# Kernel optimization log

Hardware: AMD Instinct MI355X
Metric: run time of the kernel (lower is better)

The kernel has to match this reference:

```python
import jax, jax.numpy as jnp
import numpy as np

B = 64          # graphs per batch
NN = 4096       # nodes per graph (64x64 lattice)
N = B * NN      # total nodes
DEG = 4         # avg degree
E = N * DEG     # total directed edges
DIN, H, L = 1, 128, 64


def setup_inputs() -> dict:
    key = jax.random.key(0)
    ks = jax.random.split(key, 16)
    x = jax.random.normal(ks[0], (N, DIN), dtype=jnp.float32)
    eps = jax.random.normal(ks[1], (B, L), dtype=jnp.float32)
    # per-graph random edges, offset so they never cross graphs
    src = jax.random.randint(ks[2], (E,), 0, NN)
    dst = jax.random.randint(ks[3], (E,), 0, NN)
    off = (jnp.arange(E) // (NN * DEG)) * NN
    edge_index = jnp.stack([src + off, dst + off]).astype(jnp.int32)
    batch = (jnp.arange(N) // NN).astype(jnp.int32)
    s = 0.02
    p = lambda k, shp: s * jax.random.normal(k, shp, dtype=jnp.float32)
    return {
        "x": x, "eps": eps,
        "enc_w1": p(ks[4], (DIN, H)), "enc_b1": jnp.zeros((H,), jnp.float32),
        "enc_w2": p(ks[5], (H, H)),   "enc_b2": jnp.zeros((H,), jnp.float32),
        "mu_w": p(ks[6], (H, L)),     "mu_b": jnp.zeros((L,), jnp.float32),
        "lv_w": p(ks[7], (H, L)),     "lv_b": jnp.zeros((L,), jnp.float32),
        "zn_w": p(ks[8], (L, H)),     "zn_b": jnp.zeros((H,), jnp.float32),
        "dec_w1": p(ks[9], (H, H)),   "dec_b1": jnp.zeros((H,), jnp.float32),
        "dec_w2": p(ks[10], (H, H)),  "dec_b2": jnp.zeros((H,), jnp.float32),
        "out_w": p(ks[11], (H, 1)),   "out_b": jnp.zeros((1,), jnp.float32),
        "edge_index": edge_index, "batch": batch,
    }


def _gcn(h, w, b, row, col, norm, n):
    # PyG GCNConv: xW -> gather at row, scale by sym-norm, scatter-sum at col, + bias
    hw = h @ w
    msg = hw[row] * norm[:, None]
    return jax.ops.segment_sum(msg, col, num_segments=n) + b


def reference(x, eps, enc_w1, enc_b1, enc_w2, enc_b2, mu_w, mu_b, lv_w, lv_b,
              zn_w, zn_b, dec_w1, dec_b1, dec_w2, dec_b2, out_w, out_b,
              edge_index, batch):
    n = x.shape[0]
    b = eps.shape[0]
    nn_ = n // b
    # add self-loops, symmetric GCN normalization (shared by all convs)
    loops = jnp.arange(n, dtype=edge_index.dtype)
    row = jnp.concatenate([edge_index[0], loops])
    col = jnp.concatenate([edge_index[1], loops])
    deg = jax.ops.segment_sum(jnp.ones_like(col, dtype=x.dtype), col, num_segments=n)
    dinv = jnp.where(deg > 0, jax.lax.rsqrt(deg), 0.0)
    norm = dinv[row] * dinv[col]
    h = jax.nn.relu(_gcn(x, enc_w1, enc_b1, row, col, norm, n))
    h = jax.nn.relu(_gcn(h, enc_w2, enc_b2, row, col, norm, n))
    cnt = jax.ops.segment_sum(jnp.ones((n,), x.dtype), batch, num_segments=b)
    hg = jax.ops.segment_sum(h, batch, num_segments=b) / cnt[:, None]
    mu = hg @ mu_w + mu_b
    logvar = hg @ lv_w + lv_b
    # ---- reparameterize ----
    z = mu + jnp.exp(0.5 * logvar) * eps
    zn = z @ zn_w + zn_b          # [B, H]
    hd = zn[batch]                # [N, H]
    hd = jax.nn.relu(_gcn(hd, dec_w1, dec_b1, row, col, norm, n))
    hd = jax.nn.relu(_gcn(hd, dec_w2, dec_b2, row, col, norm, n))
    spin = jnp.tanh(hd @ out_w + out_b)   # [N, 1]
    recon = spin.reshape(b, nn_)
    return (recon, mu, logvar, z)
```

## Files before the change

kernel.cpp:

```cpp
#include <hip/hip_runtime.h>
#include <math.h>

#define NTOT 262144
#define BG   64
#define NNPG 4096
#define ET   1048576
#define EPG  16384
#define EPB  4096
#define HD   128
#define LD   64
#define NSEG 129
#define TN   256
#define MCAP ET

__device__ __forceinline__ void swz(int b, int& g, int& j){
  int xcd = b & 7, q = b >> 3;
  g = (q >> 2)*8 + xcd;
  j = q & 3;
}

__global__ void __launch_bounds__(1024) k_count(const int* __restrict__ ei,
                                                int* __restrict__ cntJ){
  __shared__ int h[NNPG];
  int g, j; swz(blockIdx.x, g, j);
  int tid = threadIdx.x;
  #pragma unroll
  for (int k = tid; k < NNPG; k += 1024) h[k] = 0;
  __syncthreads();
  int gbase = g*NNPG;
  const int4* dsts4 = (const int4*)(ei + ET + g*EPG + j*EPB);
  int4 D = dsts4[tid];
  atomicAdd(&h[D.x - gbase], 1); atomicAdd(&h[D.y - gbase], 1);
  atomicAdd(&h[D.z - gbase], 1); atomicAdd(&h[D.w - gbase], 1);
  __syncthreads();
  int* plane = cntJ + j*NTOT + gbase;
  #pragma unroll
  for (int k = tid; k < NNPG; k += 1024) plane[k] = h[k];
}

__global__ void k_dinvxd(const int* __restrict__ cntJ, const float* __restrict__ x,
                         float2* __restrict__ xd){
  int i = blockIdx.x*256 + threadIdx.x;
  int deg = cntJ[i] + cntJ[NTOT+i] + cntJ[2*NTOT+i] + cntJ[3*NTOT+i];
  xd[i] = make_float2(x[i], rsqrtf((float)deg + 1.0f));
}

__global__ void __launch_bounds__(128) k_tab1a(
    const float* __restrict__ w1, const float* __restrict__ b1,
    float* __restrict__ t1, int* __restrict__ nfp){
  __shared__ int ks[128];
  int j = threadIdx.x;
  float w = w1[j], b = b1[j];
  float t; int kind;
  if (w != 0.0f){ t = -b / w; kind = (w > 0.0f) ? 0 : 1; }
  else          { t = INFINITY; kind = 2; }
  ks[j] = kind;
  t1[j] = t;
  __syncthreads();
  if (j == 0){
    int c = 0;
    for (int q = 0; q < 128; q++) c += (ks[q] != 2) ? 1 : 0;
    nfp[0] = c;
  }
}

__global__ void __launch_bounds__(1024) k_edge1(
    const int* __restrict__ ei, const float2* __restrict__ xd,
    float2* __restrict__ accJ)
{
  __shared__ float ax[NNPG];
  __shared__ float s1[NNPG];
  int tid = threadIdx.x;
  int g, j; swz(blockIdx.x, g, j);
  int gbase = g*NNPG;
  const int4* srcs4 = (const int4*)(ei + g*EPG + j*EPB);
  const int4* dsts4 = (const int4*)(ei + ET + g*EPG + j*EPB);
  int4 S = srcs4[tid], D = dsts4[tid];
  *(float4*)(ax + 4*tid) = make_float4(0.f,0.f,0.f,0.f);
  *(float4*)(s1 + 4*tid) = make_float4(0.f,0.f,0.f,0.f);
  __syncthreads();
  #define P1(s_, d_) { float2 sd = xd[s_]; int dl = (d_) - gbase; \
    atomicAdd(&ax[dl], sd.y * sd.x); \
    atomicAdd(&s1[dl], sd.y); }
  P1(S.x, D.x); P1(S.y, D.y); P1(S.z, D.z); P1(S.w, D.w);
  #undef P1
  __syncthreads();
  float4* ap = (float4*)(accJ + (size_t)j*NTOT + gbase);
  ap[2*tid+0] = make_float4(ax[4*tid+0], s1[4*tid+0], ax[4*tid+1], s1[4*tid+1]);
  ap[2*tid+1] = make_float4(ax[4*tid+2], s1[4*tid+2], ax[4*tid+3], s1[4*tid+3]);
}

__global__ void k_pack(const float2* __restrict__ xd, const float2* __restrict__ accJ,
                       const float* __restrict__ t1,
                       float4* __restrict__ rec, float* __restrict__ srowA,
                       int* __restrict__ segU1){
  __shared__ float ts[128];
  __shared__ int used[8];
  int tid = threadIdx.x;
  if (tid < 128) ts[tid] = t1[tid];
  if (tid < 8) used[tid] = 0;
  __syncthreads();
  int i = blockIdx.x*256 + tid;
  float2 xdv = xd[i];
  float2 a0 = accJ[0*NTOT + i], a1 = accJ[1*NTOT + i];
  float2 a2 = accJ[2*NTOT + i], a3 = accJ[3*NTOT + i];
  float axs = (a0.x + a1.x) + (a2.x + a3.x);
  float s1s = (a0.y + a1.y) + (a2.y + a3.y);
  float di = xdv.y;
  float ax = di * (di * xdv.x + axs);
  float sr = di * (di + s1s);
  int sc = 0;
  for (int q = 0; q < 128; q++) sc += (ts[q] < ax) ? 1 : 0;
  rec[i] = make_float4(di, di*ax, di*sr, __int_as_float(sc));
  srowA[i] = sr;
  atomicOr(&used[sc>>5], 1u << (sc & 31));
  __syncthreads();
  if (tid < 8 && used[tid]) atomicOr(&segU1[tid], used[tid]);
}

__global__ void __launch_bounds__(1024) k_tabrows(
    const float* __restrict__ wsrc, const float* __restrict__ bsrc,
    const float* __restrict__ w2, const int* __restrict__ segUsed,
    const int* __restrict__ nfA, float* __restrict__ ACbase)
{
  __shared__ float ws[128], bs[128], tsh[128];
  __shared__ int ks[128], rr[128];
  __shared__ float red[8][128][4];
  int g = blockIdx.x;
  int tid = threadIdx.x;
  int k = tid & 127, qg = tid >> 7;
  if (qg == 0){
    float w = wsrc[g*HD + k], b = bsrc[k];
    float t; int kind;
    if (w != 0.0f){ t = -b / w; kind = (w > 0.0f) ? 0 : 1; }
    else          { t = INFINITY; kind = 2; }
    ws[k] = w; bs[k] = b; tsh[k] = t; ks[k] = kind;
  }
  __syncthreads();
  if (qg == 0){
    float t = tsh[k];
    int r = 0;
    for (int q = 0; q < 128; q++){
      if (ks[q] != 2){
        float tq = tsh[q];
        if (tq < t || (tq == t && q < k)) r++;
      }
    }
    rr[k] = r;
  }
  float a0=0.f, c0=0.f, an=0.f, cn=0.f;
  #pragma unroll
  for (int u = 0; u < 16; u++){
    int q = qg*16 + u;
    float v = w2[q*HD + k];
    int kd = ks[q];
    float wq = ws[q], bq = bs[q];
    bool m0 = (kd == 1) || (kd == 2 && bq > 0.f);
    bool mn = (kd == 0) || (kd == 2 && bq > 0.f);
    float wv = wq*v, bv = bq*v;
    a0 += m0 ? wv : 0.f; c0 += m0 ? bv : 0.f;
    an += mn ? wv : 0.f; cn += mn ? bv : 0.f;
  }
  red[qg][k][0]=a0; red[qg][k][1]=c0; red[qg][k][2]=an; red[qg][k][3]=cn;
  __syncthreads();
  int nf = nfA[g];
  float* ACg = ACbase + (size_t)g*NSEG*256;
  int base = (k>>2)*8 + (k&3);
  if (qg == 0){
    float A0=0.f,C0=0.f,An=0.f,Cn=0.f;
    #pragma unroll
    for (int p = 0; p < 8; p++){
      A0+=red[p][k][0]; C0+=red[p][k][1]; An+=red[p][k][2]; Cn+=red[p][k][3];
    }
    ACg[base] = A0; ACg[base+4] = C0;
    ACg[(size_t)nf*256 + base] = An; ACg[(size_t)nf*256 + base + 4] = Cn;
  }
  __syncthreads();
  for (int wd = 0; wd < 5; wd++){
    unsigned m = (unsigned)segUsed[g*8 + wd];
    if (wd == 0) m &= ~1u;
    if ((nf >> 5) == wd) m &= ~(1u << (nf & 31));
    while (m){
      int bit = __ffs(m) - 1;
      m &= m - 1;
      int s = wd*32 + bit;
      float pa=0.f, pc=0.f;
      #pragma unroll
      for (int u = 0; u < 16; u++){
        int q = qg*16 + u;
        int kd = ks[q];
        bool act = (kd == 0) ? (rr[q] < s) : (kd == 1) ? (rr[q] >= s) : (bs[q] > 0.f);
        float v = act ? w2[q*HD + k] : 0.f;
        pa = fmaf(ws[q], v, pa); pc = fmaf(bs[q], v, pc);
      }
      red[qg][k][0]=pa; red[qg][k][1]=pc;
      __syncthreads();
      if (qg == 0){
        float A=0.f,C=0.f;
        #pragma unroll
        for (int p = 0; p < 8; p++){ A+=red[p][k][0]; C+=red[p][k][1]; }
        ACg[(size_t)s*256 + base] = A; ACg[(size_t)s*256 + base + 4] = C;
      }
      __syncthreads();
    }
  }
}

__global__ void __launch_bounds__(1024) k_edge2enc(
    const int* __restrict__ ei, const float4* __restrict__ rec,
    const int* __restrict__ nfp, float4* __restrict__ sums4,
    int2* __restrict__ missL, int* __restrict__ mcnt)
{
  __shared__ float sf[NNPG*4];
  int g, j; swz(blockIdx.x, g, j);
  int tid = threadIdx.x;
  int gbase = g*NNPG;
  int nf = nfp[0];
  const int4* srcs4 = (const int4*)(ei + g*EPG + j*EPB);
  const int4* dsts4 = (const int4*)(ei + ET + g*EPG + j*EPB);
  int4 S = srcs4[tid], D = dsts4[tid];
  float4* sf4 = (float4*)sf;
  #pragma unroll
  for (int k = 0; k < 4; k++) sf4[4*tid + k] = make_float4(0.f,0.f,0.f,0.f);
  __syncthreads();
  #define E1(s_, d_) { float4 r = rec[s_]; int dl = (d_) - gbase; \
    int sb = __float_as_int(r.w); \
    atomicAdd(&sf[dl*4+0], r.y); atomicAdd(&sf[dl*4+1], r.x); \
    if (sb == nf) { atomicAdd(&sf[dl*4+2], r.y); atomicAdd(&sf[dl*4+3], r.x); } \
    else if (sb != 0) { int ix = atomicAdd(&mcnt[0], 1); \
      if (ix < MCAP) missL[ix] = make_int2(d_, s_); } }
  E1(S.x, D.x); E1(S.y, D.y); E1(S.z, D.z); E1(S.w, D.w);
  #undef E1
  __syncthreads();
  float4* sp = sums4 + (size_t)j*NTOT + gbase;
  #pragma unroll
  for (int k = 0; k < 4; k++) sp[4*tid + k] = sf4[4*tid + k];
}

__global__ void __launch_bounds__(256) k_enc_fin(
    const float4* __restrict__ rec, const float4* __restrict__ sums4,
    const float4* __restrict__ AC, const float* __restrict__ b2,
    const int* __restrict__ nfp, const int2* __restrict__ missL,
    const int* __restrict__ mcnt, float* __restrict__ hgsum)
{
  __shared__ float4 sS[TN];
  __shared__ float4 sRA[TN];
  __shared__ float red[256*4];
  int bid = blockIdx.x, g = bid & 63, part = bid >> 6;
  int tid = threadIdx.x, lane = tid & 31, nrow = tid >> 5;
  int base = g*NNPG + part*TN;
  int nf = nfp[0];
  {
    int i = base + tid;
    sRA[tid] = rec[i];
    float4 a = sums4[0*NTOT + i], b = sums4[1*NTOT + i];
    float4 c = sums4[2*NTOT + i], d = sums4[3*NTOT + i];
    sS[tid] = make_float4(a.x+b.x+c.x+d.x, a.y+b.y+c.y+d.y,
                          a.z+b.z+c.z+d.z, a.w+b.w+c.w+d.w);
  }
  __syncthreads();
  const float4* q0 = AC + (size_t)lane*2;
  const float4* qn = AC + ((size_t)nf*32 + lane)*2;
  float4 A0 = q0[0], C0 = q0[1], An = qn[0], Cn = qn[1];
  float4 dA = make_float4(An.x-A0.x, An.y-A0.y, An.z-A0.z, An.w-A0.w);
  float4 dC = make_float4(Cn.x-C0.x, Cn.y-C0.y, Cn.z-C0.z, Cn.w-C0.w);
  float4 bb = ((const float4*)b2)[lane];
  int mc = mcnt[0]; mc = mc < MCAP ? mc : MCAP;
  float gx=0.f, gy=0.f, gz=0.f, gw=0.f;
  for (int it = 0; it < TN/8; ++it){
    int li = it*8 + nrow;
    int i = base + li;
    float4 rA = sRA[li];
    float4 s4 = sS[li];
    float accx = fmaf(s4.x,A0.x, fmaf(s4.z,dA.x, fmaf(s4.y,C0.x, s4.w*dC.x)));
    float accy = fmaf(s4.x,A0.y, fmaf(s4.z,dA.y, fmaf(s4.y,C0.y, s4.w*dC.y)));
    float accz = fmaf(s4.x,A0.z, fmaf(s4.z,dA.z, fmaf(s4.y,C0.z, s4.w*dC.z)));
    float accw = fmaf(s4.x,A0.w, fmaf(s4.z,dA.w, fmaf(s4.y,C0.w, s4.w*dC.w)));
    if (mc > 0){
      for (int e = 0; e < mc; e++){
        int2 me = missL[e];
        if (me.x == i){
          float4 r = rec[me.y];
          int sb = __float_as_int(r.w);
          const float4* qm = AC + ((size_t)sb*32 + lane)*2;
          float4 qa = qm[0], qc = qm[1];
          accx = fmaf(r.y, qa.x-A0.x, fmaf(r.x, qc.x-C0.x, accx));
          accy = fmaf(r.y, qa.y-A0.y, fmaf(r.x, qc.y-C0.y, accy));
          accz = fmaf(r.y, qa.z-A0.z, fmaf(r.x, qc.z-C0.z, accz));
          accw = fmaf(r.y, qa.w-A0.w, fmaf(r.x, qc.w-C0.w, accw));
        }
      }
    }
    int si = __float_as_int(rA.w);
    bool m0 = (si == 0);
    float4 sa, sc;
    sa.x = m0 ? A0.x : An.x; sa.y = m0 ? A0.y : An.y; sa.z = m0 ? A0.z : An.z; sa.w = m0 ? A0.w : An.w;
    sc.x = m0 ? C0.x : Cn.x; sc.y = m0 ? C0.y : Cn.y; sc.z = m0 ? C0.z : Cn.z; sc.w = m0 ? C0.w : Cn.w;
    if (si != 0 && si != nf){
      const float4* qs = AC + ((size_t)si*32 + lane)*2;
      sa = qs[0]; sc = qs[1];
    }
    float d = rA.x, d2 = d*d, ca = rA.y*d;
    gx += fmaxf(fmaf(d, accx, fmaf(ca, sa.x, d2*sc.x)) + bb.x, 0.f);
    gy += fmaxf(fmaf(d, accy, fmaf(ca, sa.y, d2*sc.y)) + bb.y, 0.f);
    gz += fmaxf(fmaf(d, accz, fmaf(ca, sa.z, d2*sc.z)) + bb.z, 0.f);
    gw += fmaxf(fmaf(d, accw, fmaf(ca, sa.w, d2*sc.w)) + bb.w, 0.f);
  }
  __syncthreads();
  red[tid*4+0] = gx; red[tid*4+1] = gy; red[tid*4+2] = gz; red[tid*4+3] = gw;
  __syncthreads();
  if (nrow == 0){
    float tx=0.f, ty=0.f, tz=0.f, tw=0.f;
    for (int r2 = 0; r2 < 8; r2++){
      int t2 = (r2*32 + lane)*4;
      tx += red[t2]; ty += red[t2+1]; tz += red[t2+2]; tw += red[t2+3];
    }
    atomicAdd(&hgsum[g*HD + lane*4 + 0], tx);
    atomicAdd(&hgsum[g*HD + lane*4 + 1], ty);
    atomicAdd(&hgsum[g*HD + lane*4 + 2], tz);
    atomicAdd(&hgsum[g*HD + lane*4 + 3], tw);
  }
}

__global__ void __launch_bounds__(128) k_small(
    const float* __restrict__ hgsum,
    const float* __restrict__ mu_w, const float* __restrict__ mu_b,
    const float* __restrict__ lv_w, const float* __restrict__ lv_b,
    const float* __restrict__ eps,
    const float* __restrict__ zn_w, const float* __restrict__ zn_b,
    const float* __restrict__ dec_w1, const float* __restrict__ dec_b1,
    float* __restrict__ out_mu, float* __restrict__ out_lv, float* __restrict__ out_z,
    float* __restrict__ t2, float* __restrict__ ushG, int* __restrict__ nf2)
{
  int g = blockIdx.x, tid = threadIdx.x;
  __shared__ float hg[128], zsh[64], znsh[128];
  __shared__ int ks[128];
  hg[tid] = hgsum[g*HD + tid] * (1.0f/4096.0f);
  __syncthreads();
  if (tid < 64){
    int l = tid;
    float m = mu_b[l], v = lv_b[l];
    for (int k = 0; k < HD; k++){
      float hv = hg[k];
      m = fmaf(hv, mu_w[k*LD + l], m);
      v = fmaf(hv, lv_w[k*LD + l], v);
    }
    int o = g*LD + l;
    out_mu[o] = m; out_lv[o] = v;
    float zv = fmaf(expf(0.5f*v), eps[o], m);
    out_z[o] = zv; zsh[l] = zv;
  }
  __syncthreads();
  {
    int k = tid;
    float acc = zn_b[k];
    for (int l = 0; l < LD; l++) acc = fmaf(zsh[l], zn_w[l*HD + k], acc);
    znsh[k] = acc;
  }
  __syncthreads();
  float w;
  {
    int k = tid;
    float acc = 0.f;
    for (int j = 0; j < HD; j++) acc = fmaf(znsh[j], dec_w1[j*HD + k], acc);
    ushG[g*HD + k] = acc;
    w = acc;
  }
  float b = dec_b1[tid];
  float t; int kind;
  if (w != 0.0f){ t = -b / w; kind = (w > 0.0f) ? 0 : 1; }
  else          { t = INFINITY; kind = 2; }
  t2[g*HD + tid] = t; ks[tid] = kind;
  __syncthreads();
  if (tid == 0){
    int c = 0;
    for (int q = 0; q < 128; q++) c += (ks[q] != 2) ? 1 : 0;
    nf2[g] = c;
  }
}

__global__ void k_seg2(const float* __restrict__ t2, const float* __restrict__ srowA,
                       float4* __restrict__ rec, int* __restrict__ segUsed){
  __shared__ float ts[128];
  __shared__ int used[8];
  int tid = threadIdx.x;
  int i = blockIdx.x*256 + tid;
  int g = blockIdx.x >> 4;
  if (tid < 128) ts[tid] = t2[g*HD + tid];
  if (tid < 8) used[tid] = 0;
  __syncthreads();
  float a = srowA[i];
  int sc = 0;
  for (int q = 0; q < 128; q++) sc += (ts[q] < a) ? 1 : 0;
  float4 r = rec[i];
  r.y = __int_as_float(sc);
  rec[i] = r;
  atomicOr(&used[sc>>5], 1u << (sc & 31));
  __syncthreads();
  if (tid < 8 && used[tid]) atomicOr(&segUsed[g*8 + tid], used[tid]);
}

__global__ void __launch_bounds__(1024) k_edge2dec(
    const int* __restrict__ ei, const float4* __restrict__ rec,
    const int* __restrict__ nf2, float4* __restrict__ sums4,
    int2* __restrict__ missL, int* __restrict__ mcnt)
{
  __shared__ float sf[NNPG*4];
  int g, j; swz(blockIdx.x, g, j);
  int tid = threadIdx.x;
  int gbase = g*NNPG;
  int nf = nf2[g];
  const int4* srcs4 = (const int4*)(ei + g*EPG + j*EPB);
  const int4* dsts4 = (const int4*)(ei + ET + g*EPG + j*EPB);
  int4 S = srcs4[tid], D = dsts4[tid];
  float4* sf4 = (float4*)sf;
  #pragma unroll
  for (int k = 0; k < 4; k++) sf4[4*tid + k] = make_float4(0.f,0.f,0.f,0.f);
  __syncthreads();
  #define E2(s_, d_) { float4 r = rec[s_]; int dl = (d_) - gbase; \
    int sb = __float_as_int(r.y); \
    atomicAdd(&sf[dl*4+0], r.z); atomicAdd(&sf[dl*4+1], r.x); \
    if (sb == nf) { atomicAdd(&sf[dl*4+2], r.z); atomicAdd(&sf[dl*4+3], r.x); } \
    else if (sb != 0) { int ix = atomicAdd(&mcnt[1], 1); \
      if (ix < MCAP) missL[ix] = make_int2(d_, s_); } }
  E2(S.x, D.x); E2(S.y, D.y); E2(S.z, D.z); E2(S.w, D.w);
  #undef E2
  __syncthreads();
  float4* sp = sums4 + (size_t)j*NTOT + gbase;
  #pragma unroll
  for (int k = 0; k < 4; k++) sp[4*tid + k] = sf4[4*tid + k];
}

__global__ void __launch_bounds__(256) k_dec_fin(
    const float4* __restrict__ rec, const float4* __restrict__ sums4,
    const float4* __restrict__ AC2, const float* __restrict__ b2,
    const float* __restrict__ ow, const float* __restrict__ ob,
    const int* __restrict__ nf2, const int2* __restrict__ missL,
    const int* __restrict__ mcnt, float* __restrict__ recon)
{
  __shared__ float4 sS[TN];
  __shared__ float4 sRA[TN];
  int bid = blockIdx.x, g = bid & 63, part = bid >> 6;
  int tid = threadIdx.x, lane = tid & 31, nrow = tid >> 5;
  int base = g*NNPG + part*TN;
  int nf = nf2[g];
  const float4* AC = AC2 + (size_t)g*NSEG*64;
  {
    int i = base + tid;
    sRA[tid] = rec[i];
    float4 a = sums4[0*NTOT + i], b = sums4[1*NTOT + i];
    float4 c = sums4[2*NTOT + i], d = sums4[3*NTOT + i];
    sS[tid] = make_float4(a.x+b.x+c.x+d.x, a.y+b.y+c.y+d.y,
                          a.z+b.z+c.z+d.z, a.w+b.w+c.w+d.w);
  }
  __syncthreads();
  const float4* q0 = AC + (size_t)lane*2;
  const float4* qn = AC + ((size_t)nf*32 + lane)*2;
  float4 A0 = q0[0], C0 = q0[1], An = qn[0], Cn = qn[1];
  float4 dA = make_float4(An.x-A0.x, An.y-A0.y, An.z-A0.z, An.w-A0.w);
  float4 dC = make_float4(Cn.x-C0.x, Cn.y-C0.y, Cn.z-C0.z, Cn.w-C0.w);
  float4 bb  = ((const float4*)b2)[lane];
  float4 owv = ((const float4*)ow)[lane];
  float obv = ob[0];
  int mc = mcnt[1]; mc = mc < MCAP ? mc : MCAP;
  for (int it = 0; it < TN/8; ++it){
    int li = it*8 + nrow;
    int i = base + li;
    float4 rA = sRA[li];
    float4 s4 = sS[li];
    float accx = fmaf(s4.x,A0.x, fmaf(s4.z,dA.x, fmaf(s4.y,C0.x, s4.w*dC.x)));
    float accy = fmaf(s4.x,A0.y, fmaf(s4.z,dA.y, fmaf(s4.y,C0.y, s4.w*dC.y)));
    float accz = fmaf(s4.x,A0.z, fmaf(s4.z,dA.z, fmaf(s4.y,C0.z, s4.w*dC.z)));
    float accw = fmaf(s4.x,A0.w, fmaf(s4.z,dA.w, fmaf(s4.y,C0.w, s4.w*dC.w)));
    if (mc > 0){
      for (int e = 0; e < mc; e++){
        int2 me = missL[e];
        if (me.x == i){
          float4 r = rec[me.y];
          int sb = __float_as_int(r.y);
          const float4* qm = AC + ((size_t)sb*32 + lane)*2;
          float4 qa = qm[0], qc = qm[1];
          accx = fmaf(r.z, qa.x-A0.x, fmaf(r.x, qc.x-C0.x, accx));
          accy = fmaf(r.z, qa.y-A0.y, fmaf(r.x, qc.y-C0.y, accy));
          accz = fmaf(r.z, qa.z-A0.z, fmaf(r.x, qc.z-C0.z, accz));
          accw = fmaf(r.z, qa.w-A0.w, fmaf(r.x, qc.w-C0.w, accw));
        }
      }
    }
    int si = __float_as_int(rA.y);
    bool m0 = (si == 0);
    float4 sa, sc;
    sa.x = m0 ? A0.x : An.x; sa.y = m0 ? A0.y : An.y; sa.z = m0 ? A0.z : An.z; sa.w = m0 ? A0.w : An.w;
    sc.x = m0 ? C0.x : Cn.x; sc.y = m0 ? C0.y : Cn.y; sc.z = m0 ? C0.z : Cn.z; sc.w = m0 ? C0.w : Cn.w;
    if (si != 0 && si != nf){
      const float4* qs = AC + ((size_t)si*32 + lane)*2;
      sa = qs[0]; sc = qs[1];
    }
    float d = rA.x, d2 = d*d, ca = rA.z*d;
    float hx = fmaxf(fmaf(d, accx, fmaf(ca, sa.x, d2*sc.x)) + bb.x, 0.f);
    float hy = fmaxf(fmaf(d, accy, fmaf(ca, sa.y, d2*sc.y)) + bb.y, 0.f);
    float hz = fmaxf(fmaf(d, accz, fmaf(ca, sa.z, d2*sc.z)) + bb.z, 0.f);
    float hw = fmaxf(fmaf(d, accw, fmaf(ca, sa.w, d2*sc.w)) + bb.w, 0.f);
    float dsum = hx*owv.x + hy*owv.y + hz*owv.z + hw*owv.w;
    for (int o2 = 16; o2 > 0; o2 >>= 1) dsum += __shfl_down(dsum, o2, 32);
    if (lane == 0) recon[i] = tanhf(dsum + obv);
  }
}

extern "C" void kernel_launch(void* const* d_in, const int* in_sizes, int n_in,
                              void* d_out, int out_size, void* d_ws, size_t ws_size,
                              hipStream_t stream){
  (void)in_sizes; (void)n_in; (void)out_size; (void)ws_size;
  const float* x      = (const float*)d_in[0];
  const float* eps    = (const float*)d_in[1];
  const float* enc_w1 = (const float*)d_in[2];
  const float* enc_b1 = (const float*)d_in[3];
  const float* enc_w2 = (const float*)d_in[4];
  const float* enc_b2 = (const float*)d_in[5];
  const float* mu_w   = (const float*)d_in[6];
  const float* mu_b   = (const float*)d_in[7];
  const float* lv_w   = (const float*)d_in[8];
  const float* lv_b   = (const float*)d_in[9];
  const float* zn_w   = (const float*)d_in[10];
  const float* zn_b   = (const float*)d_in[11];
  const float* dec_w1 = (const float*)d_in[12];
  const float* dec_b1 = (const float*)d_in[13];
  const float* dec_w2 = (const float*)d_in[14];
  const float* dec_b2 = (const float*)d_in[15];
  const float* out_w  = (const float*)d_in[16];
  const float* out_b  = (const float*)d_in[17];
  const int*   ei     = (const int*)d_in[18];

  float* out       = (float*)d_out;
  float* out_recon = out;
  float* out_mu    = out + NTOT;
  float* out_lv    = out_mu + BG*LD;
  float* out_z     = out_lv + BG*LD;

  char* w = (char*)d_ws;
  size_t off_b = 0;
  auto alloc = [&](size_t bytes)->void*{
    void* p = w + off_b;
    off_b += (bytes + 255) & ~(size_t)255;
    return p;
  };
  char*   regA   = (char*) alloc((size_t)4*NTOT*16);
  int*    cntJ   = (int*)   regA;
  float2* accJ   = (float2*)(regA + (size_t)4*NTOT*4);
  float4* sums4  = (float4*)regA;
  float2* xd     = (float2*)alloc((size_t)NTOT*8);
  float4* rec    = (float4*)alloc((size_t)NTOT*16);
  float*  srowA  = (float*) alloc((size_t)NTOT*4);
  int2*   missL  = (int2*)  alloc((size_t)MCAP*8);
  float*  t1     = (float*) alloc(128*4);
  int*    nf1    = (int*)   alloc(256);
  int*    nf2    = (int*)   alloc(BG*4);
  int*    segU1  = (int*)   alloc(8*4);
  int*    segU   = (int*)   alloc(BG*8*4);
  float*  t2     = (float*) alloc((size_t)BG*HD*4);
  float*  ushG   = (float*) alloc((size_t)BG*HD*4);
  float*  AC1    = (float*) alloc((size_t)NSEG*256*4);
  float*  AC2    = (float*) alloc((size_t)BG*NSEG*256*4);
  float*  hgsum  = (float*) alloc((size_t)BG*HD*4 + 256);
  int*    mcnt   = (int*)(hgsum + BG*HD);

  hipMemsetAsync(hgsum, 0, (size_t)BG*HD*4 + 256, stream);
  hipMemsetAsync(segU1, 0, 8*4, stream);
  hipMemsetAsync(segU,  0, (size_t)BG*8*4, stream);

  k_tab1a <<<1, 128, 0, stream>>>(enc_w1, enc_b1, t1, nf1);
  k_count <<<256, 1024, 0, stream>>>(ei, cntJ);
  k_dinvxd<<<NTOT/256, 256, 0, stream>>>(cntJ, x, xd);
  k_edge1 <<<256, 1024, 0, stream>>>(ei, xd, accJ);
  k_pack  <<<NTOT/256, 256, 0, stream>>>(xd, accJ, t1, rec, srowA, segU1);
  k_tabrows<<<1, 1024, 0, stream>>>(enc_w1, enc_b1, enc_w2, segU1, nf1, AC1);

  k_edge2enc<<<256, 1024, 0, stream>>>(ei, rec, nf1, sums4, missL, mcnt);
  k_enc_fin <<<1024, 256, 0, stream>>>(rec, sums4, (const float4*)AC1, enc_b2,
                                       nf1, missL, mcnt, hgsum);

  k_small<<<BG, 128, 0, stream>>>(hgsum, mu_w, mu_b, lv_w, lv_b, eps,
                                  zn_w, zn_b, dec_w1, dec_b1,
                                  out_mu, out_lv, out_z, t2, ushG, nf2);

  k_seg2<<<NTOT/256, 256, 0, stream>>>(t2, srowA, rec, segU);

  k_tabrows<<<BG, 1024, 0, stream>>>(ushG, dec_b1, dec_w2, segU, nf2, AC2);

  k_edge2dec<<<256, 1024, 0, stream>>>(ei, rec, nf2, sums4, missL, mcnt);
  k_dec_fin <<<1024, 256, 0, stream>>>(rec, sums4, (const float4*)AC2, dec_b2,
                                       out_w, out_b, nf2, missL, mcnt, out_recon);
}
```

Measured before the change: 177.9 us.

## Fuse setup memsets and small kernels, stage per-graph node records in LDS

```diff
diff --git a/kernel.cpp b/kernel.cpp
--- a/kernel.cpp
+++ b/kernel.cpp
@@ -20,10 +20,36 @@
 }
 
 __global__ void __launch_bounds__(1024) k_count(const int* __restrict__ ei,
-                                                int* __restrict__ cntJ){
+                                                const float* __restrict__ w1,
+                                                const float* __restrict__ b1,
+                                                int* __restrict__ cntJ,
+                                                float* __restrict__ t1, int* __restrict__ nfp,
+                                                float* __restrict__ hgsum,
+                                                int* __restrict__ mcnt,
+                                                int* __restrict__ segU1){
   __shared__ int h[NNPG];
+  int tid = threadIdx.x;
+  if (blockIdx.x == 256){
+    for (int idx = tid; idx < BG*HD; idx += 1024) hgsum[idx] = 0.f;
+    if (tid < 2) mcnt[tid] = 0;
+    if (tid < 8) segU1[tid] = 0;
+    if (tid < 128){
+      float w = w1[tid], b = b1[tid];
+      float t; int kind;
+      if (w != 0.0f){ t = -b / w; kind = (w > 0.0f) ? 0 : 1; }
+      else          { t = INFINITY; kind = 2; }
+      h[tid] = kind;
+      t1[tid] = t;
+    }
+    __syncthreads();
+    if (tid == 0){
+      int c = 0;
+      for (int q = 0; q < 128; q++) c += (h[q] != 2) ? 1 : 0;
+      nfp[0] = c;
+    }
+    return;
+  }
   int g, j; swz(blockIdx.x, g, j);
-  int tid = threadIdx.x;
   #pragma unroll
   for (int k = tid; k < NNPG; k += 1024) h[k] = 0;
   __syncthreads();
@@ -43,25 +69,6 @@
   int i = blockIdx.x*256 + threadIdx.x;
   int deg = cntJ[i] + cntJ[NTOT+i] + cntJ[2*NTOT+i] + cntJ[3*NTOT+i];
   xd[i] = make_float2(x[i], rsqrtf((float)deg + 1.0f));
-}
-
-__global__ void __launch_bounds__(128) k_tab1a(
-    const float* __restrict__ w1, const float* __restrict__ b1,
-    float* __restrict__ t1, int* __restrict__ nfp){
-  __shared__ int ks[128];
-  int j = threadIdx.x;
-  float w = w1[j], b = b1[j];
-  float t; int kind;
-  if (w != 0.0f){ t = -b / w; kind = (w > 0.0f) ? 0 : 1; }
-  else          { t = INFINITY; kind = 2; }
-  ks[j] = kind;
-  t1[j] = t;
-  __syncthreads();
-  if (j == 0){
-    int c = 0;
-    for (int q = 0; q < 128; q++) c += (ks[q] != 2) ? 1 : 0;
-    nfp[0] = c;
-  }
 }
 
 __global__ void __launch_bounds__(1024) k_edge1(
@@ -212,6 +219,7 @@
     int2* __restrict__ missL, int* __restrict__ mcnt)
 {
   __shared__ float sf[NNPG*4];
+  __shared__ float4 sRec[NNPG];
   int g, j; swz(blockIdx.x, g, j);
   int tid = threadIdx.x;
   int gbase = g*NNPG;
@@ -221,9 +229,12 @@
   int4 S = srcs4[tid], D = dsts4[tid];
   float4* sf4 = (float4*)sf;
   #pragma unroll
-  for (int k = 0; k < 4; k++) sf4[4*tid + k] = make_float4(0.f,0.f,0.f,0.f);
-  __syncthreads();
-  #define E1(s_, d_) { float4 r = rec[s_]; int dl = (d_) - gbase; \
+  for (int k = 0; k < 4; k++){
+    sf4[4*tid + k] = make_float4(0.f,0.f,0.f,0.f);
+    sRec[k*1024 + tid] = rec[gbase + k*1024 + tid];
+  }
+  __syncthreads();
+  #define E1(s_, d_) { float4 r = sRec[(s_) - gbase]; int dl = (d_) - gbase; \
     int sb = __float_as_int(r.w); \
     atomicAdd(&sf[dl*4+0], r.y); atomicAdd(&sf[dl*4+1], r.x); \
     if (sb == nf) { atomicAdd(&sf[dl*4+2], r.y); atomicAdd(&sf[dl*4+3], r.x); } \
@@ -322,20 +333,24 @@
   }
 }
 
-__global__ void __launch_bounds__(128) k_small(
+__global__ void __launch_bounds__(1024) k_small(
     const float* __restrict__ hgsum,
     const float* __restrict__ mu_w, const float* __restrict__ mu_b,
     const float* __restrict__ lv_w, const float* __restrict__ lv_b,
     const float* __restrict__ eps,
     const float* __restrict__ zn_w, const float* __restrict__ zn_b,
     const float* __restrict__ dec_w1, const float* __restrict__ dec_b1,
+    const float* __restrict__ srowA,
     float* __restrict__ out_mu, float* __restrict__ out_lv, float* __restrict__ out_z,
-    float* __restrict__ t2, float* __restrict__ ushG, int* __restrict__ nf2)
+    float* __restrict__ ushG, int* __restrict__ nf2,
+    float4* __restrict__ rec, int* __restrict__ segUsed)
 {
   int g = blockIdx.x, tid = threadIdx.x;
   __shared__ float hg[128], zsh[64], znsh[128];
-  __shared__ int ks[128];
-  hg[tid] = hgsum[g*HD + tid] * (1.0f/4096.0f);
+  __shared__ float ts[128];
+  __shared__ int ks[128], used[8];
+  if (tid < 128) hg[tid] = hgsum[g*HD + tid] * (1.0f/4096.0f);
+  if (tid < 8) used[tid] = 0;
   __syncthreads();
   if (tid < 64){
     int l = tid;
@@ -351,53 +366,42 @@
     out_z[o] = zv; zsh[l] = zv;
   }
   __syncthreads();
-  {
-    int k = tid;
-    float acc = zn_b[k];
-    for (int l = 0; l < LD; l++) acc = fmaf(zsh[l], zn_w[l*HD + k], acc);
-    znsh[k] = acc;
-  }
-  __syncthreads();
-  float w;
-  {
-    int k = tid;
+  if (tid < 128){
+    float acc = zn_b[tid];
+    for (int l = 0; l < LD; l++) acc = fmaf(zsh[l], zn_w[l*HD + tid], acc);
+    znsh[tid] = acc;
+  }
+  __syncthreads();
+  if (tid < 128){
     float acc = 0.f;
-    for (int j = 0; j < HD; j++) acc = fmaf(znsh[j], dec_w1[j*HD + k], acc);
-    ushG[g*HD + k] = acc;
-    w = acc;
-  }
-  float b = dec_b1[tid];
-  float t; int kind;
-  if (w != 0.0f){ t = -b / w; kind = (w > 0.0f) ? 0 : 1; }
-  else          { t = INFINITY; kind = 2; }
-  t2[g*HD + tid] = t; ks[tid] = kind;
+    for (int j = 0; j < HD; j++) acc = fmaf(znsh[j], dec_w1[j*HD + tid], acc);
+    ushG[g*HD + tid] = acc;
+    float b = dec_b1[tid];
+    float t; int kind;
+    if (acc != 0.0f){ t = -b / acc; kind = (acc > 0.0f) ? 0 : 1; }
+    else            { t = INFINITY; kind = 2; }
+    ts[tid] = t; ks[tid] = kind;
+  }
   __syncthreads();
   if (tid == 0){
     int c = 0;
     for (int q = 0; q < 128; q++) c += (ks[q] != 2) ? 1 : 0;
     nf2[g] = c;
   }
-}
-
-__global__ void k_seg2(const float* __restrict__ t2, const float* __restrict__ srowA,
-                       float4* __restrict__ rec, int* __restrict__ segUsed){
-  __shared__ float ts[128];
-  __shared__ int used[8];
-  int tid = threadIdx.x;
-  int i = blockIdx.x*256 + tid;
-  int g = blockIdx.x >> 4;
-  if (tid < 128) ts[tid] = t2[g*HD + tid];
-  if (tid < 8) used[tid] = 0;
-  __syncthreads();
-  float a = srowA[i];
-  int sc = 0;
-  for (int q = 0; q < 128; q++) sc += (ts[q] < a) ? 1 : 0;
-  float4 r = rec[i];
-  r.y = __int_as_float(sc);
-  rec[i] = r;
-  atomicOr(&used[sc>>5], 1u << (sc & 31));
-  __syncthreads();
-  if (tid < 8 && used[tid]) atomicOr(&segUsed[g*8 + tid], used[tid]);
+  int gbase = g*NNPG;
+  #pragma unroll
+  for (int q = 0; q < 4; q++){
+    int i = gbase + q*1024 + tid;
+    float a = srowA[i];
+    int sc = 0;
+    for (int qq = 0; qq < 128; qq++) sc += (ts[qq] < a) ? 1 : 0;
+    float4 r = rec[i];
+    r.y = __int_as_float(sc);
+    rec[i] = r;
+    atomicOr(&used[sc>>5], 1u << (sc & 31));
+  }
+  __syncthreads();
+  if (tid < 8) segUsed[g*8 + tid] = used[tid];
 }
 
 __global__ void __launch_bounds__(1024) k_edge2dec(
@@ -406,6 +410,7 @@
     int2* __restrict__ missL, int* __restrict__ mcnt)
 {
   __shared__ float sf[NNPG*4];
+  __shared__ float4 sRec[NNPG];
   int g, j; swz(blockIdx.x, g, j);
   int tid = threadIdx.x;
   int gbase = g*NNPG;
@@ -415,9 +420,12 @@
   int4 S = srcs4[tid], D = dsts4[tid];
   float4* sf4 = (float4*)sf;
   #pragma unroll
-  for (int k = 0; k < 4; k++) sf4[4*tid + k] = make_float4(0.f,0.f,0.f,0.f);
-  __syncthreads();
-  #define E2(s_, d_) { float4 r = rec[s_]; int dl = (d_) - gbase; \
+  for (int k = 0; k < 4; k++){
+    sf4[4*tid + k] = make_float4(0.f,0.f,0.f,0.f);
+    sRec[k*1024 + tid] = rec[gbase + k*1024 + tid];
+  }
+  __syncthreads();
+  #define E2(s_, d_) { float4 r = sRec[(s_) - gbase]; int dl = (d_) - gbase; \
     int sb = __float_as_int(r.y); \
     atomicAdd(&sf[dl*4+0], r.z); atomicAdd(&sf[dl*4+1], r.x); \
     if (sb == nf) { atomicAdd(&sf[dl*4+2], r.z); atomicAdd(&sf[dl*4+3], r.x); } \
@@ -557,19 +565,15 @@
   int*    nf2    = (int*)   alloc(BG*4);
   int*    segU1  = (int*)   alloc(8*4);
   int*    segU   = (int*)   alloc(BG*8*4);
-  float*  t2     = (float*) alloc((size_t)BG*HD*4);
   float*  ushG   = (float*) alloc((size_t)BG*HD*4);
   float*  AC1    = (float*) alloc((size_t)NSEG*256*4);
   float*  AC2    = (float*) alloc((size_t)BG*NSEG*256*4);
-  float*  hgsum  = (float*) alloc((size_t)BG*HD*4 + 256);
-  int*    mcnt   = (int*)(hgsum + BG*HD);
-
-  hipMemsetAsync(hgsum, 0, (size_t)BG*HD*4 + 256, stream);
-  hipMemsetAsync(segU1, 0, 8*4, stream);
-  hipMemsetAsync(segU,  0, (size_t)BG*8*4, stream);
-
-  k_tab1a <<<1, 128, 0, stream>>>(enc_w1, enc_b1, t1, nf1);
-  k_count <<<256, 1024, 0, stream>>>(ei, cntJ);
+  float*  hgsum  = (float*) alloc((size_t)BG*HD*4);
+  int*    mcnt   = (int*)   alloc(256);
+
+
+  k_count <<<257, 1024, 0, stream>>>(ei, enc_w1, enc_b1, cntJ, t1, nf1,
+                                     hgsum, mcnt, segU1);
   k_dinvxd<<<NTOT/256, 256, 0, stream>>>(cntJ, x, xd);
   k_edge1 <<<256, 1024, 0, stream>>>(ei, xd, accJ);
   k_pack  <<<NTOT/256, 256, 0, stream>>>(xd, accJ, t1, rec, srowA, segU1);
@@ -579,11 +583,9 @@
   k_enc_fin <<<1024, 256, 0, stream>>>(rec, sums4, (const float4*)AC1, enc_b2,
                                        nf1, missL, mcnt, hgsum);
 
-  k_small<<<BG, 128, 0, stream>>>(hgsum, mu_w, mu_b, lv_w, lv_b, eps,
-                                  zn_w, zn_b, dec_w1, dec_b1,
-                                  out_mu, out_lv, out_z, t2, ushG, nf2);
-
-  k_seg2<<<NTOT/256, 256, 0, stream>>>(t2, srowA, rec, segU);
+  k_small<<<BG, 1024, 0, stream>>>(hgsum, mu_w, mu_b, lv_w, lv_b, eps,
+                                   zn_w, zn_b, dec_w1, dec_b1, srowA,
+                                   out_mu, out_lv, out_z, ushG, nf2, rec, segU);
 
   k_tabrows<<<BG, 1024, 0, stream>>>(ushG, dec_b1, dec_w2, segU, nf2, AC2);
 
```

Result: slower. 206.7 us (+16.2%).

## Fold memsets and threshold setup into count kernel; stage rec in LDS

Applied to the files above, without the earlier changes.

```diff
diff --git a/kernel.cpp b/kernel.cpp
--- a/kernel.cpp
+++ b/kernel.cpp
@@ -20,10 +20,38 @@
 }
 
 __global__ void __launch_bounds__(1024) k_count(const int* __restrict__ ei,
-                                                int* __restrict__ cntJ){
+                                                const float* __restrict__ w1,
+                                                const float* __restrict__ b1,
+                                                int* __restrict__ cntJ,
+                                                float* __restrict__ t1, int* __restrict__ nfp,
+                                                float* __restrict__ hgsum,
+                                                int* __restrict__ mcnt,
+                                                int* __restrict__ segU1,
+                                                int* __restrict__ segU){
   __shared__ int h[NNPG];
+  int tid = threadIdx.x;
+  if (blockIdx.x == 256){
+    for (int idx = tid; idx < BG*HD; idx += 1024) hgsum[idx] = 0.f;
+    if (tid < 2) mcnt[tid] = 0;
+    if (tid < 8) segU1[tid] = 0;
+    if (tid < BG*8) segU[tid] = 0;
+    if (tid < 128){
+      float w = w1[tid], b = b1[tid];
+      float t; int kind;
+      if (w != 0.0f){ t = -b / w; kind = (w > 0.0f) ? 0 : 1; }
+      else          { t = INFINITY; kind = 2; }
+      h[tid] = kind;
+      t1[tid] = t;
+    }
+    __syncthreads();
+    if (tid == 0){
+      int c = 0;
+      for (int q = 0; q < 128; q++) c += (h[q] != 2) ? 1 : 0;
+      nfp[0] = c;
+    }
+    return;
+  }
   int g, j; swz(blockIdx.x, g, j);
-  int tid = threadIdx.x;
   #pragma unroll
   for (int k = tid; k < NNPG; k += 1024) h[k] = 0;
   __syncthreads();
@@ -43,25 +71,6 @@
   int i = blockIdx.x*256 + threadIdx.x;
   int deg = cntJ[i] + cntJ[NTOT+i] + cntJ[2*NTOT+i] + cntJ[3*NTOT+i];
   xd[i] = make_float2(x[i], rsqrtf((float)deg + 1.0f));
-}
-
-__global__ void __launch_bounds__(128) k_tab1a(
-    const float* __restrict__ w1, const float* __restrict__ b1,
-    float* __restrict__ t1, int* __restrict__ nfp){
-  __shared__ int ks[128];
-  int j = threadIdx.x;
-  float w = w1[j], b = b1[j];
-  float t; int kind;
-  if (w != 0.0f){ t = -b / w; kind = (w > 0.0f) ? 0 : 1; }
-  else          { t = INFINITY; kind = 2; }
-  ks[j] = kind;
-  t1[j] = t;
-  __syncthreads();
-  if (j == 0){
-    int c = 0;
-    for (int q = 0; q < 128; q++) c += (ks[q] != 2) ? 1 : 0;
-    nfp[0] = c;
-  }
 }
 
 __global__ void __launch_bounds__(1024) k_edge1(
@@ -212,6 +221,7 @@
     int2* __restrict__ missL, int* __restrict__ mcnt)
 {
   __shared__ float sf[NNPG*4];
+  __shared__ float4 sRec[NNPG];
   int g, j; swz(blockIdx.x, g, j);
   int tid = threadIdx.x;
   int gbase = g*NNPG;
@@ -221,9 +231,12 @@
   int4 S = srcs4[tid], D = dsts4[tid];
   float4* sf4 = (float4*)sf;
   #pragma unroll
-  for (int k = 0; k < 4; k++) sf4[4*tid + k] = make_float4(0.f,0.f,0.f,0.f);
-  __syncthreads();
-  #define E1(s_, d_) { float4 r = rec[s_]; int dl = (d_) - gbase; \
+  for (int k = 0; k < 4; k++){
+    sf4[4*tid + k] = make_float4(0.f,0.f,0.f,0.f);
+    sRec[k*1024 + tid] = rec[gbase + k*1024 + tid];
+  }
+  __syncthreads();
+  #define E1(s_, d_) { float4 r = sRec[(s_) - gbase]; int dl = (d_) - gbase; \
     int sb = __float_as_int(r.w); \
     atomicAdd(&sf[dl*4+0], r.y); atomicAdd(&sf[dl*4+1], r.x); \
     if (sb == nf) { atomicAdd(&sf[dl*4+2], r.y); atomicAdd(&sf[dl*4+3], r.x); } \
@@ -406,6 +419,7 @@
     int2* __restrict__ missL, int* __restrict__ mcnt)
 {
   __shared__ float sf[NNPG*4];
+  __shared__ float4 sRec[NNPG];
   int g, j; swz(blockIdx.x, g, j);
   int tid = threadIdx.x;
   int gbase = g*NNPG;
@@ -415,9 +429,12 @@
   int4 S = srcs4[tid], D = dsts4[tid];
   float4* sf4 = (float4*)sf;
   #pragma unroll
-  for (int k = 0; k < 4; k++) sf4[4*tid + k] = make_float4(0.f,0.f,0.f,0.f);
-  __syncthreads();
-  #define E2(s_, d_) { float4 r = rec[s_]; int dl = (d_) - gbase; \
+  for (int k = 0; k < 4; k++){
+    sf4[4*tid + k] = make_float4(0.f,0.f,0.f,0.f);
+    sRec[k*1024 + tid] = rec[gbase + k*1024 + tid];
+  }
+  __syncthreads();
+  #define E2(s_, d_) { float4 r = sRec[(s_) - gbase]; int dl = (d_) - gbase; \
     int sb = __float_as_int(r.y); \
     atomicAdd(&sf[dl*4+0], r.z); atomicAdd(&sf[dl*4+1], r.x); \
     if (sb == nf) { atomicAdd(&sf[dl*4+2], r.z); atomicAdd(&sf[dl*4+3], r.x); } \
@@ -561,15 +578,12 @@
   float*  ushG   = (float*) alloc((size_t)BG*HD*4);
   float*  AC1    = (float*) alloc((size_t)NSEG*256*4);
   float*  AC2    = (float*) alloc((size_t)BG*NSEG*256*4);
-  float*  hgsum  = (float*) alloc((size_t)BG*HD*4 + 256);
-  int*    mcnt   = (int*)(hgsum + BG*HD);
-
-  hipMemsetAsync(hgsum, 0, (size_t)BG*HD*4 + 256, stream);
-  hipMemsetAsync(segU1, 0, 8*4, stream);
-  hipMemsetAsync(segU,  0, (size_t)BG*8*4, stream);
-
-  k_tab1a <<<1, 128, 0, stream>>>(enc_w1, enc_b1, t1, nf1);
-  k_count <<<256, 1024, 0, stream>>>(ei, cntJ);
+  float*  hgsum  = (float*) alloc((size_t)BG*HD*4);
+  int*    mcnt   = (int*)   alloc(256);
+
+
+  k_count <<<257, 1024, 0, stream>>>(ei, enc_w1, enc_b1, cntJ, t1, nf1,
+                                     hgsum, mcnt, segU1, segU);
   k_dinvxd<<<NTOT/256, 256, 0, stream>>>(cntJ, x, xd);
   k_edge1 <<<256, 1024, 0, stream>>>(ei, xd, accJ);
   k_pack  <<<NTOT/256, 256, 0, stream>>>(xd, accJ, t1, rec, srowA, segU1);
```

Result: faster. 168.5 us (-5.3%).
